# Optimization experiments

Hardware: AMD Instinct MI355X
Metric: run time of the kernel (lower is better)

## Reference

```python
import jax, jax.numpy as jnp
import numpy as np
from jax import lax

T, B = 128, 32
V, H = 50257, 512


def _leaky(x, beta):
    # StateLeaky leaky integrator: mem[t] = beta * mem[t-1] + x[t], mem[-1] = 0.
    # x: [T, B, H], beta: [H] (broadcast per-channel decay)
    def step(mem, xt):
        mem = beta * mem + xt
        return mem, mem
    _, mem = lax.scan(step, jnp.zeros_like(x[0]), x)
    return mem  # [T, B, H]


def setup_inputs() -> dict:
    key = jax.random.key(0)
    ks = jax.random.split(key, 10)
    s_emb = 1.0  # nn.Embedding default init N(0,1)
    lim = 1.0 / np.sqrt(H)  # nn.Linear default U(-1/sqrt(fan_in), 1/sqrt(fan_in))
    return {
        "x": jax.random.randint(ks[0], (T, B), 0, V, dtype=jnp.int64),
        "emb": jax.random.normal(ks[1], (V, H), jnp.float32) * s_emb,
        "pos_emb": jax.random.normal(ks[2], (T, H), jnp.float32) * s_emb,
        "beta1": jnp.full((H,), 0.9, jnp.float32),
        "beta2": jnp.full((H,), 0.9, jnp.float32),
        "beta3": jnp.full((H,), 0.9, jnp.float32),
        "fc2_w": jax.random.uniform(ks[3], (H, H), jnp.float32, -lim, lim),
        "fc2_b": jax.random.uniform(ks[4], (H,), jnp.float32, -lim, lim),
        "fc3_w": jax.random.uniform(ks[5], (H, H), jnp.float32, -lim, lim),
        "fc3_b": jax.random.uniform(ks[6], (H,), jnp.float32, -lim, lim),
        "fco_w": jax.random.uniform(ks[7], (V, H), jnp.float32, -lim, lim),
        "fco_b": jax.random.uniform(ks[8], (V,), jnp.float32, -lim, lim),
    }


def reference(x, emb, pos_emb, beta1, beta2, beta3, fc2_w, fc2_b, fc3_w, fc3_b, fco_w, fco_b):
    # token embed + positional embed (pos broadcast over batch dim)
    h = emb[x] + pos_emb[:, None, :]                      # [T, B, H]
    h = _leaky(h, beta1)                                  # StateLeaky 1
    h = jax.nn.relu(jnp.einsum('tbh,oh->tbo', h, fc2_w) + fc2_b)
    h = _leaky(h, beta2)                                  # StateLeaky 2
    h = jax.nn.relu(jnp.einsum('tbh,oh->tbo', h, fc3_w) + fc3_b)
    h = _leaky(h, beta3)                                  # StateLeaky 3
    out = jnp.einsum('tbh,vh->tbv', h, fco_w) + fco_b     # [T, B, V] logits
    return out
```

## Files before the change

kernel.cpp:

```cpp
#include <hip/hip_runtime.h>

typedef __attribute__((ext_vector_type(8))) short short8;
typedef __attribute__((ext_vector_type(4))) float f32x4;
typedef unsigned short u16;
typedef unsigned int u32;

#define DEVI __device__ __forceinline__

DEVI u16 f2bf(float f) {
    union { float f; u32 u; } v; v.f = f;
    u32 r = v.u + 0x7FFFu + ((v.u >> 16) & 1u);
    return (u16)(r >> 16);
}

__global__ void cvt3_kernel(const float* __restrict__ a, u16* __restrict__ oa, int na4,
                            const float* __restrict__ b, u16* __restrict__ ob, int nb4,
                            const float* __restrict__ c, u16* __restrict__ oc, int nc4) {
    int total = na4 + nb4 + nc4;
    int stride = gridDim.x * blockDim.x;
    for (int i = blockIdx.x * blockDim.x + threadIdx.x; i < total; i += stride) {
        const float* in; u16* out; int j = i;
        if (j < na4) { in = a; out = oa; }
        else if ((j -= na4) < nb4) { in = b; out = ob; }
        else { j -= nb4; in = c; out = oc; }
        float4 v = reinterpret_cast<const float4*>(in)[j];
        ushort4 o;
        o.x = f2bf(v.x); o.y = f2bf(v.y); o.z = f2bf(v.z); o.w = f2bf(v.w);
        reinterpret_cast<ushort4*>(out)[j] = o;
    }
}

__global__ __launch_bounds__(64)
void embed_leaky_kernel(const int* __restrict__ x, const float* __restrict__ emb,
                        const float* __restrict__ pos, const float* __restrict__ beta,
                        u16* __restrict__ Aout) {
    __shared__ int xs[128];
    int gtid = blockIdx.x * 64 + threadIdx.x;
    int b = gtid >> 9;
    int h = gtid & 511;
    for (int i = threadIdx.x; i < 128; i += 64) xs[i] = x[i * 32 + b];
    __syncthreads();
    float be = beta[h];
    float mem = 0.f;
    for (int t0 = 0; t0 < 128; t0 += 8) {
        float e[8];
#pragma unroll
        for (int j = 0; j < 8; ++j)
            e[j] = emb[(size_t)xs[t0 + j] * 512 + h] + pos[(t0 + j) * 512 + h];
#pragma unroll
        for (int j = 0; j < 8; ++j) {
            mem = be * mem + e[j];
            Aout[(size_t)((t0 + j) * 32 + b) * 512 + h] = f2bf(mem);
        }
    }
}

__global__ __launch_bounds__(64)
void leaky_bf16_kernel(const float* __restrict__ in, const float* __restrict__ beta,
                       u16* __restrict__ Aout) {
    int gtid = blockIdx.x * 64 + threadIdx.x;
    int b = gtid >> 9;
    int h = gtid & 511;
    float be = beta[h];
    float mem = 0.f;
    for (int t0 = 0; t0 < 128; t0 += 8) {
        float v[8];
#pragma unroll
        for (int j = 0; j < 8; ++j)
            v[j] = in[(size_t)((t0 + j) * 32 + b) * 512 + h];
#pragma unroll
        for (int j = 0; j < 8; ++j) {
            mem = be * mem + v[j];
            Aout[(size_t)((t0 + j) * 32 + b) * 512 + h] = f2bf(mem);
        }
    }
}

template<bool RELU>
__global__ __launch_bounds__(256)
void gemm_bt_128(const u16* __restrict__ A, const u16* __restrict__ B,
                 const float* __restrict__ bias, float* __restrict__ C,
                 int M, int N, int K, int tiles_n) {
    __shared__ alignas(16) char smem[32 * 132 * 4];
    u16* As = (u16*)smem;
    u16* Bs = (u16*)(smem + 8192);
    float* Ep = (float*)smem;

    const int tid = threadIdx.x;
    int bm = blockIdx.x / tiles_n;
    int bn = blockIdx.x % tiles_n;
    const int wv = tid >> 6;
    const int lane = tid & 63;
    const int wr = wv >> 1, wc = wv & 1;
    const int lrow = lane & 15;
    const int kg = lane >> 4;
    const int kgp = kg ^ ((lrow >> 1) & 3);

    f32x4 acc[4][4];
#pragma unroll
    for (int i = 0; i < 4; ++i)
#pragma unroll
        for (int j = 0; j < 4; ++j) acc[i][j] = (f32x4){0.f, 0.f, 0.f, 0.f};

    const size_t rowb = (size_t)K * 2;
    const char* Ab = (const char*)A + (size_t)(bm * 128) * rowb;
    const char* Bb = (const char*)B + (size_t)(bn * 128) * rowb;

    float bv[4];
#pragma unroll
    for (int ni = 0; ni < 4; ++ni)
        bv[ni] = bias[bn * 128 + wc * 64 + ni * 16 + lrow];

    for (int k0 = 0; k0 < K; k0 += 32) {
        int k2 = k0 << 1;
#pragma unroll
        for (int r = 0; r < 2; ++r) {
            int s = r * 256 + tid;
            int row = s >> 2;
            int k16g = (s & 3) ^ ((row >> 1) & 3);
            size_t goff = (size_t)row * rowb + k2 + k16g * 16;
            __builtin_amdgcn_global_load_lds(
                (const __attribute__((address_space(1))) void*)(Ab + goff),
                (__attribute__((address_space(3))) void*)((char*)As + s * 16), 16, 0, 0);
            __builtin_amdgcn_global_load_lds(
                (const __attribute__((address_space(1))) void*)(Bb + goff),
                (__attribute__((address_space(3))) void*)((char*)Bs + s * 16), 16, 0, 0);
        }
        __syncthreads();

        short8 a[4], b[4];
#pragma unroll
        for (int mi = 0; mi < 4; ++mi)
            a[mi] = *(const short8*)&As[(wr * 64 + mi * 16 + lrow) * 32 + kgp * 8];
#pragma unroll
        for (int ni = 0; ni < 4; ++ni)
            b[ni] = *(const short8*)&Bs[(wc * 64 + ni * 16 + lrow) * 32 + kgp * 8];
#pragma unroll
        for (int mi = 0; mi < 4; ++mi)
#pragma unroll
            for (int ni = 0; ni < 4; ++ni)
                acc[mi][ni] = __builtin_amdgcn_mfma_f32_16x16x32_bf16(a[mi], b[ni], acc[mi][ni], 0, 0, 0);
        __syncthreads();
    }

#pragma unroll
    for (int mi = 0; mi < 4; ++mi) {
#pragma unroll
        for (int ni = 0; ni < 4; ++ni) {
            int c = wc * 64 + ni * 16 + lrow;
            f32x4 v = acc[mi][ni];
#pragma unroll
            for (int j = 0; j < 4; ++j) {
                float o = v[j] + bv[ni];
                if (RELU) o = fmaxf(o, 0.f);
                Ep[(wr * 16 + kg * 4 + j) * 132 + c] = o;
            }
        }
        __syncthreads();
#pragma unroll
        for (int rr = 0; rr < 8; ++rr) {
            int rl = wv * 8 + rr;
            int grow = bm * 128 + (rl >> 4) * 64 + mi * 16 + (rl & 15);
            size_t base = (size_t)grow * N + bn * 128;
#pragma unroll
            for (int hh = 0; hh < 2; ++hh) {
                int c = hh * 64 + lane;
                C[base + c] = Ep[rl * 132 + c];
            }
        }
        if (mi < 3) __syncthreads();
    }
}

__global__ __launch_bounds__(512, 4)
void gemm_bt_v(const u16* __restrict__ A, const u16* __restrict__ B,
               const float* __restrict__ bias, float* __restrict__ C,
               int M, int N, int K, int tiles_m, int tiles_n) {
    extern __shared__ char smem[];
    float* Ep = (float*)smem;

    const int tid = threadIdx.x;
    int nwg = tiles_m * tiles_n;
    int q = nwg >> 3, r = nwg & 7;
    int xcd = blockIdx.x & 7, idx = blockIdx.x >> 3;
    int wg = (xcd < r ? xcd * (q + 1) : r * (q + 1) + (xcd - r) * q) + idx;
    int bn = wg / tiles_m;
    int bm = wg % tiles_m;

    const int wv = tid >> 6;
    const int lane = tid & 63;
    const int wr = wv >> 2;
    const int wc = wv & 3;
    const int lrow = lane & 15;
    const int kg = lane >> 4;

    f32x4 acc[4][4];
#pragma unroll
    for (int i = 0; i < 4; ++i)
#pragma unroll
        for (int j = 0; j < 4; ++j) acc[i][j] = (f32x4){0.f, 0.f, 0.f, 0.f};

    const size_t rowb = (size_t)K * 2;
    const char* Ab = (const char*)A + (size_t)(bm * 128) * rowb;
    const char* Bb = (const char*)B + (size_t)(bn * 256) * rowb;

    auto STAGE = [&](int bufi, int kk) {
        char* dA = smem + bufi * 24576;
        char* dB = dA + 8192;
        int k2 = kk << 1;
        {
            int s = tid;
            int row = s >> 2, ls = s & 3;
            __builtin_amdgcn_global_load_lds(
                (const __attribute__((address_space(1))) void*)(Ab + (size_t)row * rowb + k2 + ls * 16),
                (__attribute__((address_space(3))) void*)(dA + s * 16), 16, 0, 0);
        }
#pragma unroll
        for (int j = 0; j < 2; ++j) {
            int s = j * 512 + tid;
            int row = s >> 2, ls = s & 3;
            __builtin_amdgcn_global_load_lds(
                (const __attribute__((address_space(1))) void*)(Bb + (size_t)row * rowb + k2 + ls * 16),
                (__attribute__((address_space(3))) void*)(dB + s * 16), 16, 0, 0);
        }
    };

    auto COMPUTE = [&](int bufi) {
        const char* Ah = smem + bufi * 24576;
        const char* Bh = Ah + 8192;
        short8 a[4], b[4];
#pragma unroll
        for (int mi = 0; mi < 4; ++mi) {
            int rr = wr * 64 + mi * 16 + lrow;
            a[mi] = *(const short8*)(Ah + rr * 64 + kg * 16);
        }
#pragma unroll
        for (int ni = 0; ni < 4; ++ni) {
            int rr = wc * 64 + ni * 16 + lrow;
            b[ni] = *(const short8*)(Bh + rr * 64 + kg * 16);
        }
        __builtin_amdgcn_s_setprio(1);
#pragma unroll
        for (int mi = 0; mi < 4; ++mi)
#pragma unroll
            for (int ni = 0; ni < 4; ++ni)
                acc[mi][ni] = __builtin_amdgcn_mfma_f32_16x16x32_bf16(a[mi], b[ni], acc[mi][ni], 0, 0, 0);
        __builtin_amdgcn_s_setprio(0);
    };

    const int nt = K >> 5;
    STAGE(0, 0);
    STAGE(1, 32);

    for (int t = 0; t < nt; ++t) {
        if (t < nt - 1) asm volatile("s_waitcnt vmcnt(3)" ::: "memory");
        else            asm volatile("s_waitcnt vmcnt(0)" ::: "memory");
        __builtin_amdgcn_s_barrier();
        __builtin_amdgcn_sched_barrier(0);
        if (t + 2 < nt) STAGE((t + 2) % 3, (t + 2) << 5);
        COMPUTE(t % 3);
    }

    float bv[4];
#pragma unroll
    for (int ni = 0; ni < 4; ++ni) {
        int col = bn * 256 + wc * 64 + ni * 16 + lrow;
        bv[ni] = (col < N) ? bias[col] : 0.f;
    }
    __syncthreads();

#pragma unroll
    for (int ch = 0; ch < 4; ++ch) {
        if (wr == (ch >> 1)) {
#pragma unroll
            for (int m2 = 0; m2 < 2; ++m2) {
                int mi = (ch & 1) * 2 + m2;
#pragma unroll
                for (int ni = 0; ni < 4; ++ni) {
                    int c = wc * 64 + ni * 16 + lrow;
                    f32x4 v = acc[mi][ni];
#pragma unroll
                    for (int j = 0; j < 4; ++j)
                        Ep[(m2 * 16 + kg * 4 + j) * 260 + c] = v[j] + bv[ni];
                }
            }
        }
        __syncthreads();
#pragma unroll
        for (int rr = 0; rr < 4; ++rr) {
            int rl = wv * 4 + rr;
            int grow = bm * 128 + ch * 32 + rl;
            int gc0 = bn * 256 + lane * 4;
            f32x4 v = *(const f32x4*)&Ep[rl * 260 + lane * 4];
            if (gc0 + 3 < N) {
                __builtin_nontemporal_store(v, (f32x4*)&C[(size_t)grow * N + gc0]);
            } else {
#pragma unroll
                for (int e = 0; e < 4; ++e)
                    if (gc0 + e < N)
                        __builtin_nontemporal_store(v[e], &C[(size_t)grow * N + gc0 + e]);
            }
        }
        if (ch < 3) __syncthreads();
    }
}

extern "C" void kernel_launch(void* const* d_in, const int* in_sizes, int n_in,
                              void* d_out, int out_size, void* d_ws, size_t ws_size,
                              hipStream_t stream) {
    const int* x    = (const int*)d_in[0];
    const float* emb = (const float*)d_in[1];
    const float* pos = (const float*)d_in[2];
    const float* b1 = (const float*)d_in[3];
    const float* b2 = (const float*)d_in[4];
    const float* b3 = (const float*)d_in[5];
    const float* w2 = (const float*)d_in[6];
    const float* fb2 = (const float*)d_in[7];
    const float* w3 = (const float*)d_in[8];
    const float* fb3 = (const float*)d_in[9];
    const float* wo = (const float*)d_in[10];
    const float* fbo = (const float*)d_in[11];
    float* out = (float*)d_out;

    const int V = 50257;
    const int TN = 197;
    const int Vpad = TN * 256;

    static bool lds_cap_set = false;
    if (!lds_cap_set) {
        hipFuncSetAttribute((const void*)gemm_bt_v,
                            hipFuncAttributeMaxDynamicSharedMemorySize, 73728);
        lds_cap_set = true;
    }

    char* p = (char*)d_ws;
    u16* WO = (u16*)p;  p += (size_t)Vpad * 512 * 2;
    u16* W2 = (u16*)p;  p += (size_t)512 * 512 * 2;
    u16* W3 = (u16*)p;  p += (size_t)512 * 512 * 2;
    u16* Abf = (u16*)p; p += (size_t)4096 * 512 * 2;
    float* Hb = (float*)p;

    cvt3_kernel<<<dim3(2048), dim3(256), 0, stream>>>(
        wo, WO, V * 512 / 4, w2, W2, 512 * 512 / 4, w3, W3, 512 * 512 / 4);

    embed_leaky_kernel<<<dim3(256), dim3(64), 0, stream>>>(x, emb, pos, b1, Abf);

    gemm_bt_128<true><<<dim3(32 * 4), dim3(256), 0, stream>>>(Abf, W2, fb2, Hb, 4096, 512, 512, 4);
    leaky_bf16_kernel<<<dim3(256), dim3(64), 0, stream>>>(Hb, b2, Abf);
    gemm_bt_128<true><<<dim3(32 * 4), dim3(256), 0, stream>>>(Abf, W3, fb3, Hb, 4096, 512, 512, 4);
    leaky_bf16_kernel<<<dim3(256), dim3(64), 0, stream>>>(Hb, b3, Abf);
    gemm_bt_v<<<dim3(32 * TN), dim3(512), 73728, stream>>>(Abf, WO, fbo, out, 4096, V, 512, 32, TN);
}
```

Measured before the change: 402.5 us.

## Make output GEMM persistent with XCD-partitioned tiles and swizzled LDS reads

```diff
diff --git a/kernel.cpp b/kernel.cpp
--- a/kernel.cpp
+++ b/kernel.cpp
@@ -175,17 +175,15 @@
 __global__ __launch_bounds__(512, 4)
 void gemm_bt_v(const u16* __restrict__ A, const u16* __restrict__ B,
                const float* __restrict__ bias, float* __restrict__ C,
-               int M, int N, int K, int tiles_m, int tiles_n) {
+               int M, int N, int K) {
     extern __shared__ char smem[];
-    float* Ep = (float*)smem;
 
     const int tid = threadIdx.x;
-    int nwg = tiles_m * tiles_n;
-    int q = nwg >> 3, r = nwg & 7;
-    int xcd = blockIdx.x & 7, idx = blockIdx.x >> 3;
-    int wg = (xcd < r ? xcd * (q + 1) : r * (q + 1) + (xcd - r) * q) + idx;
-    int bn = wg / tiles_m;
-    int bm = wg % tiles_m;
+    const int xcd = blockIdx.x & 7;
+    const int slot = blockIdx.x >> 3;
+    const int xbase = xcd * 788;
+    const int ntiles = (slot < 20) ? 13 : 12;
+    const int ntot = ntiles << 4;
 
     const int wv = tid >> 6;
     const int lane = tid & 63;
@@ -193,6 +191,11 @@
     const int wc = wv & 3;
     const int lrow = lane & 15;
     const int kg = lane >> 4;
+    const int kgx = kg ^ (lrow & 3);
+
+    const size_t rowb = (size_t)K * 2;
+    const char* Abase = (const char*)A;
+    const char* Bbase = (const char*)B;
 
     f32x4 acc[4][4];
 #pragma unroll
@@ -200,44 +203,47 @@
 #pragma unroll
         for (int j = 0; j < 4; ++j) acc[i][j] = (f32x4){0.f, 0.f, 0.f, 0.f};
 
-    const size_t rowb = (size_t)K * 2;
-    const char* Ab = (const char*)A + (size_t)(bm * 128) * rowb;
-    const char* Bb = (const char*)B + (size_t)(bn * 256) * rowb;
-
-    auto STAGE = [&](int bufi, int kk) {
-        char* dA = smem + bufi * 24576;
+    auto STAGE = [&](int g, int buf) {
+        int j = g >> 4;
+        int t = xbase + (j << 6) + slot;
+        int bm = t & 31, bn = t >> 5;
+        const char* Ab = Abase + ((size_t)bm << 7) * rowb;
+        const char* Bb = Bbase + ((size_t)bn << 8) * rowb;
+        int k2 = (g & 15) << 6;
+        char* dA = smem + buf * 24576;
         char* dB = dA + 8192;
-        int k2 = kk << 1;
         {
             int s = tid;
             int row = s >> 2, ls = s & 3;
+            int gsl = ls ^ (row & 3);
             __builtin_amdgcn_global_load_lds(
-                (const __attribute__((address_space(1))) void*)(Ab + (size_t)row * rowb + k2 + ls * 16),
+                (const __attribute__((address_space(1))) void*)(Ab + (size_t)row * rowb + k2 + gsl * 16),
                 (__attribute__((address_space(3))) void*)(dA + s * 16), 16, 0, 0);
         }
 #pragma unroll
-        for (int j = 0; j < 2; ++j) {
-            int s = j * 512 + tid;
+        for (int j2 = 0; j2 < 2; ++j2) {
+            int s = j2 * 512 + tid;
             int row = s >> 2, ls = s & 3;
+            int gsl = ls ^ (row & 3);
             __builtin_amdgcn_global_load_lds(
-                (const __attribute__((address_space(1))) void*)(Bb + (size_t)row * rowb + k2 + ls * 16),
+                (const __attribute__((address_space(1))) void*)(Bb + (size_t)row * rowb + k2 + gsl * 16),
                 (__attribute__((address_space(3))) void*)(dB + s * 16), 16, 0, 0);
         }
     };
 
-    auto COMPUTE = [&](int bufi) {
-        const char* Ah = smem + bufi * 24576;
+    auto COMPUTE = [&](int buf) {
+        const char* Ah = smem + buf * 24576;
         const char* Bh = Ah + 8192;
         short8 a[4], b[4];
 #pragma unroll
         for (int mi = 0; mi < 4; ++mi) {
             int rr = wr * 64 + mi * 16 + lrow;
-            a[mi] = *(const short8*)(Ah + rr * 64 + kg * 16);
+            a[mi] = *(const short8*)(Ah + rr * 64 + kgx * 16);
         }
 #pragma unroll
         for (int ni = 0; ni < 4; ++ni) {
             int rr = wc * 64 + ni * 16 + lrow;
-            b[ni] = *(const short8*)(Bh + rr * 64 + kg * 16);
+            b[ni] = *(const short8*)(Bh + rr * 64 + kgx * 16);
         }
         __builtin_amdgcn_s_setprio(1);
 #pragma unroll
@@ -248,60 +254,87 @@
         __builtin_amdgcn_s_setprio(0);
     };
 
-    const int nt = K >> 5;
     STAGE(0, 0);
-    STAGE(1, 32);
-
-    for (int t = 0; t < nt; ++t) {
-        if (t < nt - 1) asm volatile("s_waitcnt vmcnt(3)" ::: "memory");
-        else            asm volatile("s_waitcnt vmcnt(0)" ::: "memory");
+    STAGE(1, 1);
+    __builtin_amdgcn_sched_barrier(0);
+    float bv[4];
+    {
+        int t0 = xbase + slot;
+        int bn0 = t0 >> 5;
+#pragma unroll
+        for (int ni = 0; ni < 4; ++ni) {
+            int col = bn0 * 256 + wc * 64 + ni * 16 + lrow;
+            bv[ni] = bias[col < N ? col : (N - 1)];
+        }
+    }
+    __builtin_amdgcn_sched_barrier(0);
+
+    for (int g = 0; g < ntot; ++g) {
+        int k = g & 15;
+        int bufc = g % 3;
+        if (g == ntot - 1)  asm volatile("s_waitcnt vmcnt(0)" ::: "memory");
+        else if (k <= 1)    asm volatile("s_waitcnt vmcnt(7)" ::: "memory");
+        else                asm volatile("s_waitcnt vmcnt(3)" ::: "memory");
         __builtin_amdgcn_s_barrier();
         __builtin_amdgcn_sched_barrier(0);
-        if (t + 2 < nt) STAGE((t + 2) % 3, (t + 2) << 5);
-        COMPUTE(t % 3);
-    }
-
-    float bv[4];
-#pragma unroll
-    for (int ni = 0; ni < 4; ++ni) {
-        int col = bn * 256 + wc * 64 + ni * 16 + lrow;
-        bv[ni] = (col < N) ? bias[col] : 0.f;
-    }
-    __syncthreads();
-
-#pragma unroll
-    for (int ch = 0; ch < 4; ++ch) {
-        if (wr == (ch >> 1)) {
-#pragma unroll
-            for (int m2 = 0; m2 < 2; ++m2) {
-                int mi = (ch & 1) * 2 + m2;
+        if (g + 2 < ntot) STAGE(g + 2, (g + 2) % 3);
+        COMPUTE(bufc);
+
+        if (k == 15) {
+            int j = g >> 4;
+            __builtin_amdgcn_sched_barrier(0);
+            float bvn[4];
+            {
+                int t1 = xbase + ((j + 1) << 6) + slot;
+                int bn1 = (j + 1 < ntiles) ? (t1 >> 5) : 0;
 #pragma unroll
                 for (int ni = 0; ni < 4; ++ni) {
-                    int c = wc * 64 + ni * 16 + lrow;
-                    f32x4 v = acc[mi][ni];
-#pragma unroll
-                    for (int j = 0; j < 4; ++j)
-                        Ep[(m2 * 16 + kg * 4 + j) * 260 + c] = v[j] + bv[ni];
+                    int col = bn1 * 256 + wc * 64 + ni * 16 + lrow;
+                    bvn[ni] = bias[col < N ? col : (N - 1)];
                 }
             }
-        }
-        __syncthreads();
-#pragma unroll
-        for (int rr = 0; rr < 4; ++rr) {
-            int rl = wv * 4 + rr;
-            int grow = bm * 128 + ch * 32 + rl;
-            int gc0 = bn * 256 + lane * 4;
-            f32x4 v = *(const f32x4*)&Ep[rl * 260 + lane * 4];
-            if (gc0 + 3 < N) {
-                __builtin_nontemporal_store(v, (f32x4*)&C[(size_t)grow * N + gc0]);
-            } else {
-#pragma unroll
-                for (int e = 0; e < 4; ++e)
-                    if (gc0 + e < N)
-                        __builtin_nontemporal_store(v[e], &C[(size_t)grow * N + gc0 + e]);
+            int t = xbase + (j << 6) + slot;
+            int bm = t & 31, bn = t >> 5;
+            float* Ep = (float*)(smem + bufc * 24576);
+            __syncthreads();
+#pragma unroll
+            for (int ch = 0; ch < 8; ++ch) {
+                if (wr == (ch >> 2)) {
+                    int mi = ch & 3;
+#pragma unroll
+                    for (int ni = 0; ni < 4; ++ni) {
+                        int c = wc * 64 + ni * 16 + lrow;
+                        f32x4 v = acc[mi][ni];
+#pragma unroll
+                        for (int j2 = 0; j2 < 4; ++j2)
+                            Ep[(kg * 4 + j2) * 260 + c] = v[j2] + bv[ni];
+                    }
+                }
+                __syncthreads();
+#pragma unroll
+                for (int rr = 0; rr < 2; ++rr) {
+                    int rl = wv * 2 + rr;
+                    int grow = bm * 128 + ch * 16 + rl;
+                    int gc0 = bn * 256 + lane * 4;
+                    f32x4 v = *(const f32x4*)&Ep[rl * 260 + lane * 4];
+                    if (gc0 + 3 < N) {
+                        __builtin_nontemporal_store(v, (f32x4*)&C[(size_t)grow * N + gc0]);
+                    } else {
+#pragma unroll
+                        for (int e = 0; e < 4; ++e)
+                            if (gc0 + e < N)
+                                __builtin_nontemporal_store(v[e], &C[(size_t)grow * N + gc0 + e]);
+                    }
+                }
+                if (ch < 7) __syncthreads();
             }
-        }
-        if (ch < 3) __syncthreads();
+#pragma unroll
+            for (int i = 0; i < 4; ++i)
+#pragma unroll
+                for (int j2 = 0; j2 < 4; ++j2) acc[i][j2] = (f32x4){0.f, 0.f, 0.f, 0.f};
+#pragma unroll
+            for (int ni = 0; ni < 4; ++ni) bv[ni] = bvn[ni];
+        }
     }
 }
 
@@ -349,5 +382,5 @@
     leaky_bf16_kernel<<<dim3(256), dim3(64), 0, stream>>>(Hb, b2, Abf);
     gemm_bt_128<true><<<dim3(32 * 4), dim3(256), 0, stream>>>(Abf, W3, fb3, Hb, 4096, 512, 512, 4);
     leaky_bf16_kernel<<<dim3(256), dim3(64), 0, stream>>>(Hb, b3, Abf);
-    gemm_bt_v<<<dim3(32 * TN), dim3(512), 73728, stream>>>(Abf, WO, fbo, out, 4096, V, 512, 32, TN);
-}
+    gemm_bt_v<<<dim3(512), dim3(512), 73728, stream>>>(Abf, WO, fbo, out, 4096, V, 512);
+}
```

Measured after the change: 451.8 us. 12.2% more time.
